# Kernel tuning notes

Hardware: AMD Instinct MI355X
Metric: run time of the kernel (lower is better)

Reference implementation:

```python
import jax, jax.numpy as jnp
import numpy as np

B, H, L, PRED_LEN = 512, 512, 2, 256


def setup_inputs() -> dict:
    key = jax.random.key(0)
    ks = jax.random.split(key, 12)
    s = 1.0 / np.sqrt(H)  # PyTorch LSTM init scale
    f32 = jnp.float32
    return {
        "h": jax.random.normal(ks[0], (L, B, H), f32),
        "c": jax.random.normal(ks[1], (L, B, H), f32),
        "W_ih0": jax.random.normal(ks[2], (4 * H, 1), f32) * s,
        "W_hh0": jax.random.normal(ks[3], (4 * H, H), f32) * s,
        "b_ih0": jax.random.normal(ks[4], (4 * H,), f32) * s,
        "b_hh0": jax.random.normal(ks[5], (4 * H,), f32) * s,
        "W_ih1": jax.random.normal(ks[6], (4 * H, H), f32) * s,
        "W_hh1": jax.random.normal(ks[7], (4 * H, H), f32) * s,
        "b_ih1": jax.random.normal(ks[8], (4 * H,), f32) * s,
        "b_hh1": jax.random.normal(ks[9], (4 * H,), f32) * s,
        "fc_w": jax.random.normal(ks[10], (1, H), f32) * s,
        "fc_b": jax.random.normal(ks[11], (1,), f32) * s,
        "pred_len": PRED_LEN,
    }


def _lstm_cell(x, h, c, W_ih, W_hh, b_ih, b_hh):
    # PyTorch gate order: i, f, g, o
    gates = x @ W_ih.T + h @ W_hh.T + (b_ih + b_hh)
    i, f, g, o = jnp.split(gates, 4, axis=-1)
    c_new = jax.nn.sigmoid(f) * c + jax.nn.sigmoid(i) * jnp.tanh(g)
    h_new = jax.nn.sigmoid(o) * jnp.tanh(c_new)
    return h_new, c_new


def reference(h, c, W_ih0, W_hh0, b_ih0, b_hh0, W_ih1, W_hh1, b_ih1, b_hh1,
              fc_w, fc_b, pred_len):
    params = ((W_ih0, W_hh0, b_ih0, b_hh0), (W_ih1, W_hh1, b_ih1, b_hh1))
    Bsz = h.shape[1]

    def step(carry, _):
        x, hs, cs = carry  # x: (B,1); hs, cs: (L,B,H)
        inp = x
        new_h, new_c = [], []
        for l in range(len(params)):
            hn, cn = _lstm_cell(inp, hs[l], cs[l], *params[l])
            new_h.append(hn)
            new_c.append(cn)
            inp = hn
        pred = inp @ fc_w.T + fc_b  # (B,1)
        return (pred, jnp.stack(new_h), jnp.stack(new_c)), pred[:, 0]

    x0 = jnp.zeros((Bsz, 1), h.dtype)  # torch.zeros(B,1,1) start token
    _, preds = jax.lax.scan(step, (x0, h, c), None, length=pred_len)
    return preds.T  # (B, pred_len)
```

## Files before the change

kernel.cpp:

```cpp
#include <hip/hip_runtime.h>
#include <hip/hip_bf16.h>


#define B_ 512
#define H_ 512
#define T_ 256
#define NWG 256
#define NTHR 512

typedef _Float16 half8_t __attribute__((ext_vector_type(8)));
typedef _Float16 half4_t __attribute__((ext_vector_type(4)));
typedef _Float16 half2_t __attribute__((ext_vector_type(2)));
typedef float floatx4 __attribute__((ext_vector_type(4)));

#define W16_BYTES  (3u * 4u * H_ * H_ * 2u)
#define HBUF_ELEMS (B_ * H_)
#define HBUF_BYTES (HBUF_ELEMS * 2u)
#define H0_OFF   ((size_t)W16_BYTES)
#define H1_OFF   (H0_OFF + 2 * HBUF_BYTES)
#define BAR_OFF  (H1_OFF + 2 * HBUF_BYTES)
#define PART_OFF (BAR_OFF + 2048)

__device__ __forceinline__ float sigm_(float x) { return 1.0f / (1.0f + __expf(-x)); }
__device__ __forceinline__ float tanh_(float x) { return 1.0f - 2.0f / (1.0f + __expf(2.0f * x)); }

__global__ void prep_weights(const float* __restrict__ whh0,
                             const float* __restrict__ wih1,
                             const float* __restrict__ whh1,
                             _Float16* __restrict__ w16) {
    const int QM = (4 * H_ * H_) / 4;
    int i = blockIdx.x * blockDim.x + threadIdx.x;
    if (i >= 3 * QM) return;
    const float* src; int base;
    if (i < QM)          { src = whh0; base = 0; }
    else if (i < 2 * QM) { src = wih1; base = QM; }
    else                 { src = whh1; base = 2 * QM; }
    float4 v = ((const float4*)src)[i - base];
    half4_t h;
    h[0] = (_Float16)v.x; h[1] = (_Float16)v.y; h[2] = (_Float16)v.z; h[3] = (_Float16)v.w;
    ((half4_t*)w16)[i] = h;
}

__global__ void prep_state(const float* __restrict__ h_in,
                           _Float16* __restrict__ H0, _Float16* __restrict__ H1) {
    int i = blockIdx.x * blockDim.x + threadIdx.x;
    float4 a = ((const float4*)h_in)[i];
    float4 b = ((const float4*)h_in)[(B_ * H_) / 4 + i];
    half4_t ha, hb;
    ha[0] = (_Float16)a.x; ha[1] = (_Float16)a.y; ha[2] = (_Float16)a.z; ha[3] = (_Float16)a.w;
    hb[0] = (_Float16)b.x; hb[1] = (_Float16)b.y; hb[2] = (_Float16)b.z; hb[3] = (_Float16)b.w;
    ((half4_t*)H0)[i] = ha;
    ((half4_t*)H1)[i] = hb;
}

#define GLL16(gptr, lptr) __builtin_amdgcn_global_load_lds( \
    (const __attribute__((address_space(1))) unsigned int*)(gptr), \
    (__attribute__((address_space(3))) unsigned int*)(lptr), 16, 0, 0x01)

__device__ __forceinline__ void stage_rows(const char* gsrc, char* lbuf, int wv, int lane) {
#pragma unroll
    for (int i = 0; i < 8; ++i) {
        int row = wv * 8 + i;
        const char* g_ = gsrc + row * 1024 + (((lane ^ (row & 7)) & 63) << 4);
        GLL16(g_, lbuf + row * 1024);
    }
}

__device__ __forceinline__ floatx4 load16_sc0(const float* p) {
    floatx4 v;
    asm volatile("global_load_dwordx4 %0, %1, off sc0" : "=v"(v) : "v"(p) : "memory");
    return v;
}

__launch_bounds__(NTHR)
__global__ void lstm_decode(
    const float* __restrict__ c_in,
    const float* __restrict__ wih0, const float* __restrict__ bih0,
    const float* __restrict__ bhh0,
    const float* __restrict__ bih1, const float* __restrict__ bhh1,
    const float* __restrict__ fcw, const float* __restrict__ fcb,
    const _Float16* __restrict__ w16,
    _Float16* __restrict__ Hs0, _Float16* __restrict__ Hs1,
    int* __restrict__ bar, float* __restrict__ part,
    float* __restrict__ outp)
{
    __shared__ __align__(16) char bufA[65536];
    __shared__ __align__(16) char bufB[65536];
    __shared__ float gbuf[4][64][20];
    __shared__ float xrow[64];
    __shared__ int sh_bt, sh_ct;

    const int tid  = (int)threadIdx.x;
    const int lane = tid & 63;
    const int wv   = tid >> 6;
    const int g    = wv & 3;
    const int kh   = wv >> 2;
    const int cl   = lane & 15;
    const int kg   = lane >> 4;

    if (tid == 0) {
        unsigned int xcc;
        asm volatile("s_getreg_b32 %0, hwreg(HW_REG_XCC_ID)" : "=s"(xcc));
        int mybt = (int)(xcc & 7u);
        int rank = atomicAdd(&bar[256 + mybt], 1);
        sh_bt = mybt;
        sh_ct = rank & 31;
    }
    __syncthreads();
    const int bt = sh_bt;
    const int ct = sh_ct;

    const int n = g * H_ + ct * 16 + cl;
    half8_t wf0[8], wf1[8], wf2[8];
    {
        const _Float16* r0 = w16 + (size_t)n * H_ + kh * 256 + kg * 8;
        const _Float16* r1 = r0 + 4 * H_ * H_;
        const _Float16* r2 = r0 + 8 * H_ * H_;
#pragma unroll
        for (int ksg = 0; ksg < 8; ++ksg) {
            wf0[ksg] = *(const half8_t*)(r0 + ksg * 32);
            wf1[ksg] = *(const half8_t*)(r1 + ksg * 32);
            wf2[ksg] = *(const half8_t*)(r2 + ksg * 32);
        }
    }
    const float b0   = bih0[n] + bhh0[n];
    const float b1   = bih1[n] + bhh1[n];
    const float wx   = wih0[n];
    const float fcb0 = fcb[0];

    const int erow = tid >> 3;
    const int ecol = (tid & 7) * 2;
    float c0a, c0b, c1a, c1b;
    {
        size_t base0 = (size_t)(bt * 64 + erow) * H_ + ct * 16 + ecol;
        c0a = c_in[base0];                     c0b = c_in[base0 + 1];
        c1a = c_in[(size_t)B_ * H_ + base0];   c1b = c_in[(size_t)B_ * H_ + base0 + 1];
    }
    const float2 fcv = *(const float2*)(fcw + ct * 16 + ecol);

    const int abase = cl * 1024 + kh * 512 + kg * 16;
    const int axor  = (cl & 7) << 4;

    int* flagg   = bar + bt * 32;
    float* partg = part + bt * 2048;
    int ep = 0;

#define PASS(bufc, wf, acc) do {                                              \
    _Pragma("unroll")                                                         \
    for (int ksg = 0; ksg < 8; ++ksg) {                                       \
        _Pragma("unroll")                                                     \
        for (int mt = 0; mt < 4; ++mt) {                                      \
            int a_ = (abase + mt * 16384 + ksg * 64) ^ axor;                  \
            half8_t av_ = *(const half8_t*)((bufc) + a_);                     \
            acc[mt] = __builtin_amdgcn_mfma_f32_16x16x32_f16(av_, (wf)[ksg],  \
                                                             acc[mt], 0, 0, 0); \
        }                                                                     \
    }                                                                         \
} while (0)

    floatx4 accG0[4], accG1[4];
    floatx4 pv;

    if (tid < 64) xrow[tid] = 0.f;
    stage_rows((const char*)Hs0 + (size_t)bt * 64 * 1024, bufB, wv, lane);
    stage_rows((const char*)Hs1 + (size_t)bt * 64 * 1024, bufA, wv, lane);
    asm volatile("s_waitcnt vmcnt(0) lgkmcnt(0)\n\ts_barrier" ::: "memory");
#pragma unroll
    for (int mt = 0; mt < 4; ++mt) accG0[mt] = (floatx4)0.f;
    PASS(bufB, wf0, accG0);

    for (int t = 0; t < T_; ++t) {
        const size_t pnxt = (size_t)((t + 1) & 1);
        _Float16* h0w = Hs0 + pnxt * HBUF_ELEMS;
        _Float16* h1w = Hs1 + pnxt * HBUF_ELEMS;

        if (t > 0) {
            asm volatile("s_waitcnt vmcnt(8)" : "+v"(pv) :: "memory");
            float xs = (pv[0] + pv[1]) + (pv[2] + pv[3]);
            xs += __shfl_xor(xs, 1);
            xs += __shfl_xor(xs, 2);
            xs += __shfl_xor(xs, 4);
            xs += fcb0;
            if ((tid & 7) == 0) {
                xrow[tid >> 3] = xs;
                if (ct == 0) outp[(size_t)(bt * 64 + (tid >> 3)) * T_ + (t - 1)] = xs;
            }
        }
        __syncthreads();

        if (kh == 0) {
#pragma unroll
            for (int mt = 0; mt < 4; ++mt)
#pragma unroll
                for (int r = 0; r < 4; ++r)
                    gbuf[g][mt * 16 + kg * 4 + r][cl] =
                        accG0[mt][r] + __builtin_fmaf(xrow[mt * 16 + kg * 4 + r], wx, b0);
        }
        __syncthreads();
        if (kh == 1) {
#pragma unroll
            for (int mt = 0; mt < 4; ++mt)
#pragma unroll
                for (int r = 0; r < 4; ++r)
                    gbuf[g][mt * 16 + kg * 4 + r][cl] += accG0[mt][r];
        }
        __syncthreads();

        {
            float2 iv = *(const float2*)&gbuf[0][erow][ecol];
            float2 fv = *(const float2*)&gbuf[1][erow][ecol];
            float2 gv = *(const float2*)&gbuf[2][erow][ecol];
            float2 ov = *(const float2*)&gbuf[3][erow][ecol];
            float ca = sigm_(fv.x) * c0a + sigm_(iv.x) * tanh_(gv.x);
            float cb = sigm_(fv.y) * c0b + sigm_(iv.y) * tanh_(gv.y);
            c0a = ca; c0b = cb;
            half2_t hh;
            hh[0] = (_Float16)(sigm_(ov.x) * tanh_(ca));
            hh[1] = (_Float16)(sigm_(ov.y) * tanh_(cb));
            *(half2_t*)(h0w + (size_t)(bt * 64 + erow) * H_ + ct * 16 + ecol) = hh;
        }

        ++ep;
        __syncthreads();
        if (tid == 0)
            __hip_atomic_store(&flagg[ct], ep, __ATOMIC_RELAXED, __HIP_MEMORY_SCOPE_AGENT);

#pragma unroll
        for (int mt = 0; mt < 4; ++mt) {
            if (kh == 0) {
#pragma unroll
                for (int r = 0; r < 4; ++r) accG1[mt][r] = b1;
            } else {
                accG1[mt] = (floatx4)0.f;
            }
        }
        PASS(bufA, wf2, accG1);

        if (wv == 0) {
            for (;;) {
                int v_ = __hip_atomic_load(&flagg[lane & 31], __ATOMIC_RELAXED,
                                           __HIP_MEMORY_SCOPE_AGENT);
                if (__all(v_ >= ep)) break;
            }
        }
        __syncthreads();

        stage_rows((const char*)h0w + (size_t)bt * 64 * 1024, bufB, wv, lane);
        asm volatile("s_waitcnt vmcnt(0) lgkmcnt(0)\n\ts_barrier" ::: "memory");

        PASS(bufB, wf1, accG1);

        if (kh == 0) {
#pragma unroll
            for (int mt = 0; mt < 4; ++mt)
#pragma unroll
                for (int r = 0; r < 4; ++r)
                    gbuf[g][mt * 16 + kg * 4 + r][cl] = accG1[mt][r];
        }
        __syncthreads();
        if (kh == 1) {
#pragma unroll
            for (int mt = 0; mt < 4; ++mt)
#pragma unroll
                for (int r = 0; r < 4; ++r)
                    gbuf[g][mt * 16 + kg * 4 + r][cl] += accG1[mt][r];
        }
        __syncthreads();

        {
            float2 iv = *(const float2*)&gbuf[0][erow][ecol];
            float2 fv = *(const float2*)&gbuf[1][erow][ecol];
            float2 gv = *(const float2*)&gbuf[2][erow][ecol];
            float2 ov = *(const float2*)&gbuf[3][erow][ecol];
            float ca = sigm_(fv.x) * c1a + sigm_(iv.x) * tanh_(gv.x);
            float cb = sigm_(fv.y) * c1b + sigm_(iv.y) * tanh_(gv.y);
            c1a = ca; c1b = cb;
            float ha = sigm_(ov.x) * tanh_(ca);
            float hb = sigm_(ov.y) * tanh_(cb);
            half2_t hh; hh[0] = (_Float16)ha; hh[1] = (_Float16)hb;
            *(half2_t*)(h1w + (size_t)(bt * 64 + erow) * H_ + ct * 16 + ecol) = hh;
            float ps = __builtin_fmaf(ha, fcv.x, hb * fcv.y);
            ps += __shfl_xor(ps, 1);
            ps += __shfl_xor(ps, 2);
            ps += __shfl_xor(ps, 4);
            if ((tid & 7) == 0)
                partg[(tid >> 3) * 32 + ct] = ps;
        }

        ++ep;
        __syncthreads();
        if (tid == 0)
            __hip_atomic_store(&flagg[ct], ep, __ATOMIC_RELAXED, __HIP_MEMORY_SCOPE_AGENT);

#pragma unroll
        for (int mt = 0; mt < 4; ++mt) accG0[mt] = (floatx4)0.f;
        PASS(bufB, wf0, accG0);

        if (wv == 0) {
            for (;;) {
                int v_ = __hip_atomic_load(&flagg[lane & 31], __ATOMIC_RELAXED,
                                           __HIP_MEMORY_SCOPE_AGENT);
                if (__all(v_ >= ep)) break;
            }
        }
        __syncthreads();

        pv = load16_sc0(partg + (tid >> 3) * 32 + (tid & 7) * 4);
        stage_rows((const char*)Hs1 + pnxt * HBUF_BYTES + (size_t)bt * 64 * 1024,
                   bufA, wv, lane);
    }

    {
        asm volatile("s_waitcnt vmcnt(8)" : "+v"(pv) :: "memory");
        float xs = (pv[0] + pv[1]) + (pv[2] + pv[3]);
        xs += __shfl_xor(xs, 1);
        xs += __shfl_xor(xs, 2);
        xs += __shfl_xor(xs, 4);
        xs += fcb0;
        if ((tid & 7) == 0 && ct == 0)
            outp[(size_t)(bt * 64 + (tid >> 3)) * T_ + (T_ - 1)] = xs;
    }
#undef PASS
}

extern "C" void kernel_launch(void* const* d_in, const int* in_sizes, int n_in,
                              void* d_out, int out_size, void* d_ws, size_t ws_size,
                              hipStream_t stream) {
    const float* h_in = (const float*)d_in[0];
    const float* c_in = (const float*)d_in[1];
    const float* wih0 = (const float*)d_in[2];
    const float* whh0 = (const float*)d_in[3];
    const float* bih0 = (const float*)d_in[4];
    const float* bhh0 = (const float*)d_in[5];
    const float* wih1 = (const float*)d_in[6];
    const float* whh1 = (const float*)d_in[7];
    const float* bih1 = (const float*)d_in[8];
    const float* bhh1 = (const float*)d_in[9];
    const float* fcw  = (const float*)d_in[10];
    const float* fcb  = (const float*)d_in[11];
    float* out = (float*)d_out;

    char* ws = (char*)d_ws;
    _Float16* w16 = (_Float16*)ws;
    _Float16* Hs0 = (_Float16*)(ws + H0_OFF);
    _Float16* Hs1 = (_Float16*)(ws + H1_OFF);
    int* bar      = (int*)(ws + BAR_OFF);
    float* part   = (float*)(ws + PART_OFF);

    (void)hipMemsetAsync(bar, 0, 2048, stream);

    {
        const int n4 = 3 * (4 * H_ * H_) / 4;
        prep_weights<<<(n4 + 255) / 256, 256, 0, stream>>>(whh0, wih1, whh1, w16);
    }
    prep_state<<<(B_ * H_ / 4) / 256, 256, 0, stream>>>(h_in, Hs0, Hs1);

    lstm_decode<<<NWG, NTHR, 0, stream>>>(c_in, wih0, bih0, bhh0, bih1, bhh1,
                                          fcw, fcb, w16, Hs0, Hs1, bar, part, out);
}
```

Baseline: 1.815 ms.

## Split MFMA passes to overlap H staging loads and use lighter LDS barriers

Splits the layer-1 input pass and the next layer-0 recurrent pass into two halves, so half the MFMA work runs after the global-to-LDS staging is issued and hides that load latency behind compute. LDS-only synchronisation points use a barrier that waits only on lgkmcnt instead of full __syncthreads. The barriers before the flag store still wait on vmcnt so global h writes are complete first. The risk is that vmcnt(8) accounting for the pending pv load and ordering assumptions become fragile, and the extra split may add register pressure.

```diff
diff --git a/kernel.cpp b/kernel.cpp
--- a/kernel.cpp
+++ b/kernel.cpp
@@ -71,6 +71,9 @@
     asm volatile("global_load_dwordx4 %0, %1, off sc0" : "=v"(v) : "v"(p) : "memory");
     return v;
 }
+
+#define LBAR() asm volatile("s_waitcnt lgkmcnt(0)\n\ts_barrier" ::: "memory")
+#define FBAR() asm volatile("s_waitcnt vmcnt(0) lgkmcnt(0)\n\ts_barrier" ::: "memory")
 
 __launch_bounds__(NTHR)
 __global__ void lstm_decode(
@@ -145,11 +148,11 @@
     float* partg = part + bt * 2048;
     int ep = 0;
 
-#define PASS(bufc, wf, acc) do {                                              \
+#define PASSH(bufc, wf, acc, M0, M1) do {                                     \
     _Pragma("unroll")                                                         \
     for (int ksg = 0; ksg < 8; ++ksg) {                                       \
         _Pragma("unroll")                                                     \
-        for (int mt = 0; mt < 4; ++mt) {                                      \
+        for (int mt = (M0); mt <= (M1); ++mt) {                               \
             int a_ = (abase + mt * 16384 + ksg * 64) ^ axor;                  \
             half8_t av_ = *(const half8_t*)((bufc) + a_);                     \
             acc[mt] = __builtin_amdgcn_mfma_f32_16x16x32_f16(av_, (wf)[ksg],  \
@@ -164,10 +167,10 @@
     if (tid < 64) xrow[tid] = 0.f;
     stage_rows((const char*)Hs0 + (size_t)bt * 64 * 1024, bufB, wv, lane);
     stage_rows((const char*)Hs1 + (size_t)bt * 64 * 1024, bufA, wv, lane);
-    asm volatile("s_waitcnt vmcnt(0) lgkmcnt(0)\n\ts_barrier" ::: "memory");
+    FBAR();
 #pragma unroll
     for (int mt = 0; mt < 4; ++mt) accG0[mt] = (floatx4)0.f;
-    PASS(bufB, wf0, accG0);
+    PASSH(bufB, wf0, accG0, 0, 3);
 
     for (int t = 0; t < T_; ++t) {
         const size_t pnxt = (size_t)((t + 1) & 1);
@@ -186,7 +189,7 @@
                 if (ct == 0) outp[(size_t)(bt * 64 + (tid >> 3)) * T_ + (t - 1)] = xs;
             }
         }
-        __syncthreads();
+        LBAR();
 
         if (kh == 0) {
 #pragma unroll
@@ -196,7 +199,7 @@
                     gbuf[g][mt * 16 + kg * 4 + r][cl] =
                         accG0[mt][r] + __builtin_fmaf(xrow[mt * 16 + kg * 4 + r], wx, b0);
         }
-        __syncthreads();
+        LBAR();
         if (kh == 1) {
 #pragma unroll
             for (int mt = 0; mt < 4; ++mt)
@@ -204,7 +207,7 @@
                 for (int r = 0; r < 4; ++r)
                     gbuf[g][mt * 16 + kg * 4 + r][cl] += accG0[mt][r];
         }
-        __syncthreads();
+        LBAR();
 
         {
             float2 iv = *(const float2*)&gbuf[0][erow][ecol];
@@ -221,7 +224,7 @@
         }
 
         ++ep;
-        __syncthreads();
+        FBAR();
         if (tid == 0)
             __hip_atomic_store(&flagg[ct], ep, __ATOMIC_RELAXED, __HIP_MEMORY_SCOPE_AGENT);
 
@@ -234,7 +237,7 @@
                 accG1[mt] = (floatx4)0.f;
             }
         }
-        PASS(bufA, wf2, accG1);
+        PASSH(bufA, wf2, accG1, 0, 1);
 
         if (wv == 0) {
             for (;;) {
@@ -246,9 +249,12 @@
         __syncthreads();
 
         stage_rows((const char*)h0w + (size_t)bt * 64 * 1024, bufB, wv, lane);
-        asm volatile("s_waitcnt vmcnt(0) lgkmcnt(0)\n\ts_barrier" ::: "memory");
-
-        PASS(bufB, wf1, accG1);
+
+        PASSH(bufA, wf2, accG1, 2, 3);
+
+        FBAR();
+
+        PASSH(bufB, wf1, accG1, 0, 3);
 
         if (kh == 0) {
 #pragma unroll
@@ -257,7 +263,7 @@
                 for (int r = 0; r < 4; ++r)
                     gbuf[g][mt * 16 + kg * 4 + r][cl] = accG1[mt][r];
         }
-        __syncthreads();
+        LBAR();
         if (kh == 1) {
 #pragma unroll
             for (int mt = 0; mt < 4; ++mt)
@@ -265,7 +271,7 @@
                 for (int r = 0; r < 4; ++r)
                     gbuf[g][mt * 16 + kg * 4 + r][cl] += accG1[mt][r];
         }
-        __syncthreads();
+        LBAR();
 
         {
             float2 iv = *(const float2*)&gbuf[0][erow][ecol];
@@ -288,13 +294,13 @@
         }
 
         ++ep;
-        __syncthreads();
+        FBAR();
         if (tid == 0)
             __hip_atomic_store(&flagg[ct], ep, __ATOMIC_RELAXED, __HIP_MEMORY_SCOPE_AGENT);
 
 #pragma unroll
         for (int mt = 0; mt < 4; ++mt) accG0[mt] = (floatx4)0.f;
-        PASS(bufB, wf0, accG0);
+        PASSH(bufB, wf0, accG0, 0, 1);
 
         if (wv == 0) {
             for (;;) {
@@ -308,6 +314,8 @@
         pv = load16_sc0(partg + (tid >> 3) * 32 + (tid & 7) * 4);
         stage_rows((const char*)Hs1 + pnxt * HBUF_BYTES + (size_t)bt * 64 * 1024,
                    bufA, wv, lane);
+
+        PASSH(bufB, wf0, accG0, 2, 3);
     }
 
     {
@@ -320,7 +328,9 @@
         if ((tid & 7) == 0 && ct == 0)
             outp[(size_t)(bt * 64 + (tid >> 3)) * T_ + (T_ - 1)] = xs;
     }
-#undef PASS
+#undef PASSH
+#undef LBAR
+#undef FBAR
 }
 
 extern "C" void kernel_launch(void* const* d_in, const int* in_sizes, int n_in,
```

After: 1.809 ms (median of 2 runs). Within noise of the previous version (-0.3%).
